# Performance work log

Hardware: AMD Instinct MI355X
Metric: run time of the kernel (lower is better)

## Reference

```python
import jax, jax.numpy as jnp
import numpy as np

N = 50000
E = 1600000
IN = 128
HID = 128
OUT = 64
NL = 200000
NEG_SLOPE = 0.2


def _glorot(key, shape):
    fan_in, fan_out = shape[0], shape[-1]
    s = jnp.sqrt(6.0 / (fan_in + fan_out))
    return jax.random.uniform(key, shape, jnp.float32, -s, s)


def setup_inputs() -> dict:
    key = jax.random.key(0)
    ks = jax.random.split(key, 16)
    x = jax.random.normal(ks[0], (N, IN), jnp.float32)
    edge_index = jax.random.randint(ks[1], (2, E), 0, N, dtype=jnp.int32)
    edge_label_index = jax.random.randint(ks[2], (2, NL), 0, N, dtype=jnp.int32)
    return {
        "x": x,
        "edge_index": edge_index,
        "edge_label_index": edge_label_index,
        "W1": _glorot(ks[3], (IN, HID)),  "a1s": _glorot(ks[4], (HID,)),  "a1d": _glorot(ks[5], (HID,)),  "b1": jnp.zeros((HID,), jnp.float32),
        "W2": _glorot(ks[6], (HID, HID)), "a2s": _glorot(ks[7], (HID,)),  "a2d": _glorot(ks[8], (HID,)),  "b2": jnp.zeros((HID,), jnp.float32),
        "W3": _glorot(ks[9], (HID, HID)), "a3s": _glorot(ks[10], (HID,)), "a3d": _glorot(ks[11], (HID,)), "b3": jnp.zeros((HID,), jnp.float32),
        "W4": _glorot(ks[12], (HID, OUT)), "b4": jnp.zeros((OUT,), jnp.float32),
    }


def _add_self_loops(edge_index, n):
    loop = jnp.arange(n, dtype=edge_index.dtype)
    return jnp.concatenate([edge_index, jnp.stack([loop, loop])], axis=1)


def gat_conv(x, edge_index, W, a_s, a_d, b):
    """PyG GATConv, heads=1, add_self_loops=True: gather, LeakyReLU score,
    segment softmax over destination nodes, scatter-add aggregate."""
    n = x.shape[0]
    ei = _add_self_loops(edge_index, n)
    src, dst = ei[0], ei[1]
    h = x @ W                                    # [N, H]
    e = jax.nn.leaky_relu((h @ a_s)[src] + (h @ a_d)[dst], NEG_SLOPE)  # [E']
    m = jax.ops.segment_max(e, dst, num_segments=n)
    p = jnp.exp(e - m[dst])
    s = jax.ops.segment_sum(p, dst, num_segments=n)
    alpha = p / s[dst]                           # segment softmax
    out = jax.ops.segment_sum(h[src] * alpha[:, None], dst, num_segments=n)
    return out + b


def gcn_conv(x, edge_index, W, b):
    """PyG GCNConv: self-loops + symmetric degree normalization."""
    n = x.shape[0]
    ei = _add_self_loops(edge_index, n)
    src, dst = ei[0], ei[1]
    h = x @ W
    deg = jax.ops.segment_sum(jnp.ones(src.shape, h.dtype), dst, num_segments=n)
    dinv = jax.lax.rsqrt(deg)
    norm = dinv[src] * dinv[dst]                 # [E']
    out = jax.ops.segment_sum(h[src] * norm[:, None], dst, num_segments=n)
    return out + b


def reference(x, edge_index, edge_label_index,
              W1, a1s, a1d, b1, W2, a2s, a2d, b2,
              W3, a3s, a3d, b3, W4, b4):
    h = jax.nn.relu(gat_conv(x, edge_index, W1, a1s, a1d, b1))
    h = jax.nn.relu(gat_conv(h, edge_index, W2, a2s, a2d, b2))
    h = jax.nn.relu(gat_conv(h, edge_index, W3, a3s, a3d, b3))
    z = gcn_conv(h, edge_index, W4, b4)          # [N, OUT]
    # decode: dot product of endpoint embeddings -> link logits [NL]
    return (z[edge_label_index[0]] * z[edge_label_index[1]]).sum(axis=-1)
```

## Files before the change

kernel.cpp:

```cpp
#include <hip/hip_runtime.h>
#include <hip/hip_fp16.h>
#include <math.h>

#define NN   50000
#define NE   1600000
#define DHID 128
#define DOUTC 64
#define NLBL 200000
#define CAP  80
#define NEG  0.2f
#define NBK  196
#define CAPB 8800
#define CHK  4096

typedef unsigned short u16;
typedef _Float16 half8 __attribute__((ext_vector_type(8)));
typedef float floatx4 __attribute__((ext_vector_type(4)));


__global__ __launch_bounds__(256) void k_zero(int* __restrict__ gcnt) {
    int i = threadIdx.x;
    if (i < NBK) gcnt[i] = 0;
}

__global__ __launch_bounds__(256) void k_bin(const int* __restrict__ ei,
                                             int* __restrict__ gcnt,
                                             unsigned* __restrict__ bins) {
    __shared__ int cntL[NBK];
    __shared__ int curL[NBK];
    const int tid = threadIdx.x;
    const int e0 = blockIdx.x * CHK + tid * 16;
    const bool act = (e0 + 15) < NE;

    unsigned pk[16];
    int bb[16];
    if (act) {
#pragma unroll
        for (int g = 0; g < 4; ++g) {
            int4 s4 = *(const int4*)&ei[e0 + g * 4];
            int4 d4 = *(const int4*)&ei[NE + e0 + g * 4];
            int sa[4] = {s4.x, s4.y, s4.z, s4.w};
            int da[4] = {d4.x, d4.y, d4.z, d4.w};
#pragma unroll
            for (int k = 0; k < 4; ++k) {
                int idx = g * 4 + k;
                bb[idx] = da[k] >> 8;
                pk[idx] = (unsigned)sa[k] | ((unsigned)(da[k] & 255) << 16);
            }
        }
    }
    for (int i = tid; i < NBK; i += 256) cntL[i] = 0;
    __syncthreads();
    if (act) {
#pragma unroll
        for (int k = 0; k < 16; ++k) atomicAdd(&cntL[bb[k]], 1);
    }
    __syncthreads();
    for (int i = tid; i < NBK; i += 256) curL[i] = atomicAdd(&gcnt[i], cntL[i]);
    __syncthreads();
    if (act) {
#pragma unroll
        for (int k = 0; k < 16; ++k) {
            int off = atomicAdd(&curL[bb[k]], 1);
            bins[(size_t)bb[k] * CAPB + off] = pk[k];
        }
    }
}

__global__ __launch_bounds__(256) void k_build(const unsigned* __restrict__ bins,
                                               const int* __restrict__ gcnt,
                                               int* __restrict__ cnt,
                                               u16* __restrict__ csr) {
    __shared__ u16 rows[256 * CAP];
    __shared__ int cur[256];
    const int b = blockIdx.x, tid = threadIdx.x;
    const int d0 = b << 8;
    const int nd = min(256, NN - d0);
    if (tid < nd) { cur[tid] = 1; rows[tid * CAP] = (u16)(d0 + tid); }
    __syncthreads();
    const int n = gcnt[b];
    for (int i = tid; i < n; i += 256) {
        unsigned v = bins[(size_t)b * CAPB + i];
        int s = v & 0xFFFF, dl = v >> 16;
        int pos = atomicAdd(&cur[dl], 1);
        if (pos < CAP) rows[dl * CAP + pos] = (u16)s;
    }
    __syncthreads();
    const unsigned* rw = (const unsigned*)rows;
    unsigned* cw = (unsigned*)(csr + (size_t)d0 * CAP);
    const int tot = nd * (CAP / 2);
    for (int i = tid; i < tot; i += 256) cw[i] = rw[i];
    if (tid < nd) cnt[d0 + tid] = cur[tid];
}


__global__ __launch_bounds__(256) void k_cast(const float* __restrict__ x,
                                              __half* __restrict__ x16) {
    int i = (blockIdx.x * 256 + threadIdx.x) * 4;
    if (i < NN * 128) {
        float4 v = *(const float4*)&x[i];
        __half2 h0 = __floats2half2_rn(v.x, v.y);
        __half2 h1 = __floats2half2_rn(v.z, v.w);
        uint2 u;
        __builtin_memcpy(&u.x, &h0, 4);
        __builtin_memcpy(&u.y, &h1, 4);
        *(uint2*)&x16[i] = u;
    }
}


template <int NOUT, bool ATTN>
__global__ __launch_bounds__(256) void gemm_mfma(const __half* __restrict__ A16,
                                                 const float* __restrict__ W,
                                                 __half* __restrict__ C16,
                                                 const float* __restrict__ a_s,
                                                 const float* __restrict__ a_d,
                                                 float* __restrict__ asv,
                                                 float* __restrict__ adv, int M) {
    constexpr int CT = NOUT / 16;
    __shared__ _Float16 Wt[NOUT][136];
    const int tid = threadIdx.x;
    for (int i4 = tid; i4 < 128 * NOUT / 4; i4 += 256) {
        int i = i4 * 4;
        int k = i / NOUT, n = i % NOUT;
        float4 w = *(const float4*)&W[i];
        Wt[n + 0][k] = (_Float16)w.x;
        Wt[n + 1][k] = (_Float16)w.y;
        Wt[n + 2][k] = (_Float16)w.z;
        Wt[n + 3][k] = (_Float16)w.w;
    }
    __syncthreads();

    const int wave = tid >> 6, lane = tid & 63;
    const int n = lane & 15, quad = lane >> 4;
    const int row0 = blockIdx.x * 64 + wave * 16;

    half8 a[4];
    const bool rowok = (row0 + n) < M;
    const _Float16* Ap = (const _Float16*)A16 + (size_t)(row0 + n) * 128 + quad * 8;
    half8 zz = {};
#pragma unroll
    for (int ks = 0; ks < 4; ++ks)
        a[ks] = rowok ? *(const half8*)(Ap + ks * 32) : zz;

    floatx4 acc[CT];
#pragma unroll
    for (int c = 0; c < CT; ++c) acc[c] = (floatx4){0.f, 0.f, 0.f, 0.f};

#pragma unroll
    for (int c = 0; c < CT; ++c) {
#pragma unroll
        for (int ks = 0; ks < 4; ++ks) {
            half8 b = *(const half8*)&Wt[c * 16 + n][ks * 32 + quad * 8];
            acc[c] = __builtin_amdgcn_mfma_f32_16x16x32_f16(a[ks], b, acc[c], 0, 0, 0);
        }
    }

#pragma unroll
    for (int c = 0; c < CT; ++c) {
#pragma unroll
        for (int reg = 0; reg < 4; ++reg) {
            int row = row0 + quad * 4 + reg;
            if (row < M) C16[(size_t)row * NOUT + c * 16 + n] = __float2half(acc[c][reg]);
        }
    }

    if (ATTN) {
        float ps[4] = {0.f, 0.f, 0.f, 0.f};
        float pd[4] = {0.f, 0.f, 0.f, 0.f};
#pragma unroll
        for (int c = 0; c < CT; ++c) {
            float sv = a_s[c * 16 + n];
            float dv = a_d[c * 16 + n];
#pragma unroll
            for (int reg = 0; reg < 4; ++reg) {
                ps[reg] = fmaf(acc[c][reg], sv, ps[reg]);
                pd[reg] = fmaf(acc[c][reg], dv, pd[reg]);
            }
        }
#pragma unroll
        for (int off = 1; off < 16; off <<= 1) {
#pragma unroll
            for (int reg = 0; reg < 4; ++reg) {
                ps[reg] += __shfl_xor(ps[reg], off);
                pd[reg] += __shfl_xor(pd[reg], off);
            }
        }
        if (n == 0) {
#pragma unroll
            for (int reg = 0; reg < 4; ++reg) {
                int row = row0 + quad * 4 + reg;
                if (row < M) { asv[row] = ps[reg]; adv[row] = pd[reg]; }
            }
        }
    }
}

__device__ inline void fma_h8(uint4 u, float al, float* acc) {
    float2 f0 = __half22float2(*(__half2*)&u.x);
    float2 f1 = __half22float2(*(__half2*)&u.y);
    float2 f2 = __half22float2(*(__half2*)&u.z);
    float2 f3 = __half22float2(*(__half2*)&u.w);
    acc[0] = fmaf(al, f0.x, acc[0]);
    acc[1] = fmaf(al, f0.y, acc[1]);
    acc[2] = fmaf(al, f1.x, acc[2]);
    acc[3] = fmaf(al, f1.y, acc[3]);
    acc[4] = fmaf(al, f2.x, acc[4]);
    acc[5] = fmaf(al, f2.y, acc[5]);
    acc[6] = fmaf(al, f3.x, acc[6]);
    acc[7] = fmaf(al, f3.y, acc[7]);
}


__global__ __launch_bounds__(256) void k_gat_agg(const __half* __restrict__ h,
                                                 const int* __restrict__ cnt,
                                                 const u16* __restrict__ csr,
                                                 const float* __restrict__ asv,
                                                 const float* __restrict__ adv,
                                                 const float* __restrict__ bias,
                                                 __half* __restrict__ outp) {
    int lane = threadIdx.x & 63, wv = threadIdx.x >> 6;
    int d = blockIdx.x * 4 + wv;
    if (d >= NN) return;
    int deg = cnt[d]; if (deg > CAP) deg = CAP;
    const float advd = adv[d];
    const u16* rowp = csr + (size_t)d * CAP;

    int j0 = lane, j1 = lane + 64;
    int s0 = 0, s1 = 0;
    float e0 = -INFINITY, e1 = -INFINITY;
    if (j0 < deg) {
        s0 = rowp[j0];
        float t = asv[s0] + advd;
        e0 = (t >= 0.f) ? t : NEG * t;
    }
    if (j1 < deg) {
        s1 = rowp[j1];
        float t = asv[s1] + advd;
        e1 = (t >= 0.f) ? t : NEG * t;
    }
    float m = fmaxf(e0, e1);
#pragma unroll
    for (int off = 32; off; off >>= 1) m = fmaxf(m, __shfl_xor(m, off));
    float p0 = (j0 < deg) ? __expf(e0 - m) : 0.f;
    float p1 = (j1 < deg) ? __expf(e1 - m) : 0.f;
    float s = p0 + p1;
#pragma unroll
    for (int off = 32; off; off >>= 1) s += __shfl_xor(s, off);
    float inv = 1.f / s;
    float a0 = p0 * inv, a1 = p1 * inv;

    int slot = lane >> 3, r = lane & 7;
    float acc[16];
#pragma unroll
    for (int k = 0; k < 16; ++k) acc[k] = 0.f;

    for (int base = 0; base < deg; base += 8) {
        int idx = base + slot;
        int lsrc = idx & 63;
        float alA = __shfl(a0, lsrc);
        float alB = __shfl(a1, lsrc);
        int   sjA = __shfl(s0, lsrc);
        int   sjB = __shfl(s1, lsrc);
        bool ok = idx < deg;
        float al = ok ? ((idx < 64) ? alA : alB) : 0.f;
        int   sj = ok ? ((idx < 64) ? sjA : sjB) : 0;
        const uint4* hp = (const uint4*)&h[(size_t)sj * 128 + r * 16];
        uint4 ua = hp[0];
        uint4 ub = hp[1];
        fma_h8(ua, al, acc);
        fma_h8(ub, al, acc + 8);
    }
#pragma unroll
    for (int k = 0; k < 16; ++k) {
        acc[k] += __shfl_xor(acc[k], 8);
        acc[k] += __shfl_xor(acc[k], 16);
        acc[k] += __shfl_xor(acc[k], 32);
    }
    if (slot == 0) {
        __half2 ho[8];
#pragma unroll
        for (int k = 0; k < 8; ++k) {
            float oa = fmaxf(acc[2 * k]     + bias[r * 16 + 2 * k],     0.f);
            float ob = fmaxf(acc[2 * k + 1] + bias[r * 16 + 2 * k + 1], 0.f);
            ho[k] = __floats2half2_rn(oa, ob);
        }
        uint4 u0, u1;
        __builtin_memcpy(&u0, &ho[0], 16);
        __builtin_memcpy(&u1, &ho[4], 16);
        uint4* op = (uint4*)&outp[(size_t)d * 128 + r * 16];
        op[0] = u0; op[1] = u1;
    }
}


__global__ __launch_bounds__(256) void k_gcn_agg(const __half* __restrict__ h,
                                                 const int* __restrict__ cnt,
                                                 const u16* __restrict__ csr,
                                                 const float* __restrict__ bias,
                                                 float* __restrict__ z) {
    int lane = threadIdx.x & 63, wv = threadIdx.x >> 6;
    int d = blockIdx.x * 4 + wv;
    if (d >= NN) return;
    int degc = cnt[d];
    int deg = degc > CAP ? CAP : degc;
    float did = rsqrtf((float)degc);
    const u16* rowp = csr + (size_t)d * CAP;

    int j0 = lane, j1 = lane + 64;
    int s0 = 0, s1 = 0;
    float n0 = 0.f, n1 = 0.f;
    if (j0 < deg) { s0 = rowp[j0]; n0 = rsqrtf((float)cnt[s0]) * did; }
    if (j1 < deg) { s1 = rowp[j1]; n1 = rsqrtf((float)cnt[s1]) * did; }

    int slot = lane >> 3, r = lane & 7;
    float acc[8];
#pragma unroll
    for (int k = 0; k < 8; ++k) acc[k] = 0.f;

    for (int base = 0; base < deg; base += 8) {
        int idx = base + slot;
        int lsrc = idx & 63;
        float nA = __shfl(n0, lsrc);
        float nB = __shfl(n1, lsrc);
        int  sjA = __shfl(s0, lsrc);
        int  sjB = __shfl(s1, lsrc);
        bool ok = idx < deg;
        float nm = ok ? ((idx < 64) ? nA : nB) : 0.f;
        int   sj = ok ? ((idx < 64) ? sjA : sjB) : 0;
        uint4 u = *(const uint4*)&h[(size_t)sj * 64 + r * 8];
        fma_h8(u, nm, acc);
    }
#pragma unroll
    for (int k = 0; k < 8; ++k) {
        acc[k] += __shfl_xor(acc[k], 8);
        acc[k] += __shfl_xor(acc[k], 16);
        acc[k] += __shfl_xor(acc[k], 32);
    }
    if (slot == 0) {
        float4 b0 = *(const float4*)&bias[r * 8];
        float4 b1 = *(const float4*)&bias[r * 8 + 4];
        float4* zp = (float4*)&z[(size_t)d * 64 + r * 8];
        zp[0] = make_float4(acc[0] + b0.x, acc[1] + b0.y, acc[2] + b0.z, acc[3] + b0.w);
        zp[1] = make_float4(acc[4] + b1.x, acc[5] + b1.y, acc[6] + b1.z, acc[7] + b1.w);
    }
}


__global__ __launch_bounds__(256) void k_decode(const float* __restrict__ z,
                                                const int* __restrict__ eli,
                                                float* __restrict__ outp) {
    int lane = threadIdx.x & 63, wv = threadIdx.x >> 6;
    int g = lane >> 4, r = lane & 15;
    int idx = (blockIdx.x * 4 + wv) * 4 + g;
    if (idx >= NLBL) return;
    int a = eli[idx], b = eli[NLBL + idx];
    float4 za = *(const float4*)&z[(size_t)a * 64 + r * 4];
    float4 zb = *(const float4*)&z[(size_t)b * 64 + r * 4];
    float v = za.x * zb.x + za.y * zb.y + za.z * zb.z + za.w * zb.w;
#pragma unroll
    for (int off = 8; off; off >>= 1) v += __shfl_xor(v, off);
    if (r == 0) outp[idx] = v;
}


extern "C" void kernel_launch(void* const* d_in, const int* in_sizes, int n_in,
                              void* d_out, int out_size, void* d_ws, size_t ws_size,
                              hipStream_t stream) {
    const float* x   = (const float*)d_in[0];
    const int*   ei  = (const int*)d_in[1];
    const int*   eli = (const int*)d_in[2];
    const float* W1 = (const float*)d_in[3];
    const float* a1s = (const float*)d_in[4];
    const float* a1d = (const float*)d_in[5];
    const float* b1 = (const float*)d_in[6];
    const float* W2 = (const float*)d_in[7];
    const float* a2s = (const float*)d_in[8];
    const float* a2d = (const float*)d_in[9];
    const float* b2 = (const float*)d_in[10];
    const float* W3 = (const float*)d_in[11];
    const float* a3s = (const float*)d_in[12];
    const float* a3d = (const float*)d_in[13];
    const float* b3 = (const float*)d_in[14];
    const float* W4 = (const float*)d_in[15];
    const float* b4 = (const float*)d_in[16];
    float* outp = (float*)d_out;

    char* p = (char*)d_ws;
    auto alloc = [&](size_t bytes) -> char* {
        char* r = p;
        p += (bytes + 255) & ~(size_t)255;
        return r;
    };
    int*    cnt  = (int*)alloc((size_t)NN * 4);
    u16*    csr  = (u16*)alloc((size_t)NN * CAP * 2);
    int*    gcnt = (int*)alloc((size_t)NBK * 4);
    float*  asv  = (float*)alloc((size_t)NN * 4);
    float*  advv = (float*)alloc((size_t)NN * 4);
    __half* x16  = (__half*)alloc((size_t)NN * 128 * 2);
    __half* G    = (__half*)alloc((size_t)NN * 128 * 2);
    __half* Bu1  = (__half*)alloc((size_t)NN * 128 * 2);
    __half* Bu2  = (__half*)alloc((size_t)NN * 128 * 2);
    float*  zf   = (float*)alloc((size_t)NN * 64 * 4);
    unsigned* bins = (unsigned*)alloc((size_t)NBK * CAPB * 4);

    const int gBin  = (NE + CHK - 1) / CHK;
    const int gCast = (NN * 128 / 4 + 255) / 256;
    const int gGemm = (NN + 63) / 64;
    const int gNode = (NN + 3) / 4;
    const int gDec  = (NLBL + 15) / 16;

    k_zero<<<1, 256, 0, stream>>>(gcnt);
    k_bin<<<gBin, 256, 0, stream>>>(ei, gcnt, bins);
    k_build<<<NBK, 256, 0, stream>>>(bins, gcnt, cnt, csr);
    k_cast<<<gCast, 256, 0, stream>>>(x, x16);

    gemm_mfma<128, true><<<gGemm, 256, 0, stream>>>(x16, W1, G, a1s, a1d, asv, advv, NN);
    k_gat_agg<<<gNode, 256, 0, stream>>>(G, cnt, csr, asv, advv, b1, Bu1);

    gemm_mfma<128, true><<<gGemm, 256, 0, stream>>>(Bu1, W2, G, a2s, a2d, asv, advv, NN);
    k_gat_agg<<<gNode, 256, 0, stream>>>(G, cnt, csr, asv, advv, b2, Bu2);

    gemm_mfma<128, true><<<gGemm, 256, 0, stream>>>(Bu2, W3, G, a3s, a3d, asv, advv, NN);
    k_gat_agg<<<gNode, 256, 0, stream>>>(G, cnt, csr, asv, advv, b3, Bu1);

    gemm_mfma<64, false><<<gGemm, 256, 0, stream>>>(Bu1, W4, G, nullptr, nullptr, nullptr, nullptr, NN);
    k_gcn_agg<<<gNode, 256, 0, stream>>>(G, cnt, csr, b4, zf);

    k_decode<<<gDec, 256, 0, stream>>>(zf, eli, outp);
}
```

Before: 444.1 us.

## Pre-pack weights into MFMA fragment layout and double rows per wave in GEMM

```diff
diff --git a/kernel.cpp b/kernel.cpp
--- a/kernel.cpp
+++ b/kernel.cpp
@@ -109,89 +109,108 @@
 }
 
 
+__global__ __launch_bounds__(256) void k_prep_w(const float* __restrict__ W1f,
+                                                const float* __restrict__ W2f,
+                                                const float* __restrict__ W3f,
+                                                const float* __restrict__ W4f,
+                                                half8* __restrict__ Wf1,
+                                                half8* __restrict__ Wf2,
+                                                half8* __restrict__ Wf3,
+                                                half8* __restrict__ Wf4) {
+    int e = blockIdx.x * 256 + threadIdx.x;
+    const float* W;
+    half8* Wf;
+    int nout, le;
+    if (e < 2048)      { W = W1f; Wf = Wf1; nout = 128; le = e; }
+    else if (e < 4096) { W = W2f; Wf = Wf2; nout = 128; le = e - 2048; }
+    else if (e < 6144) { W = W3f; Wf = Wf3; nout = 128; le = e - 4096; }
+    else if (e < 7168) { W = W4f; Wf = Wf4; nout = 64;  le = e - 6144; }
+    else return;
+    int c = le >> 8, rem = le & 255, ks = rem >> 6, lane = rem & 63;
+    int n = lane & 15, quad = lane >> 4;
+    int col = c * 16 + n, k0 = ks * 32 + quad * 8;
+    half8 v;
+#pragma unroll
+    for (int j = 0; j < 8; ++j) v[j] = (_Float16)W[(size_t)(k0 + j) * nout + col];
+    Wf[le] = v;
+}
+
+
 template <int NOUT, bool ATTN>
 __global__ __launch_bounds__(256) void gemm_mfma(const __half* __restrict__ A16,
-                                                 const float* __restrict__ W,
+                                                 const half8* __restrict__ Wf,
                                                  __half* __restrict__ C16,
                                                  const float* __restrict__ a_s,
                                                  const float* __restrict__ a_d,
                                                  float* __restrict__ asv,
                                                  float* __restrict__ adv, int M) {
     constexpr int CT = NOUT / 16;
-    __shared__ _Float16 Wt[NOUT][136];
     const int tid = threadIdx.x;
-    for (int i4 = tid; i4 < 128 * NOUT / 4; i4 += 256) {
-        int i = i4 * 4;
-        int k = i / NOUT, n = i % NOUT;
-        float4 w = *(const float4*)&W[i];
-        Wt[n + 0][k] = (_Float16)w.x;
-        Wt[n + 1][k] = (_Float16)w.y;
-        Wt[n + 2][k] = (_Float16)w.z;
-        Wt[n + 3][k] = (_Float16)w.w;
-    }
-    __syncthreads();
-
     const int wave = tid >> 6, lane = tid & 63;
     const int n = lane & 15, quad = lane >> 4;
-    const int row0 = blockIdx.x * 64 + wave * 16;
-
-    half8 a[4];
-    const bool rowok = (row0 + n) < M;
-    const _Float16* Ap = (const _Float16*)A16 + (size_t)(row0 + n) * 128 + quad * 8;
+    const int row0 = blockIdx.x * 128 + wave * 32;
+
+    half8 a[2][4];
     half8 zz = {};
 #pragma unroll
-    for (int ks = 0; ks < 4; ++ks)
-        a[ks] = rowok ? *(const half8*)(Ap + ks * 32) : zz;
-
-    floatx4 acc[CT];
-#pragma unroll
-    for (int c = 0; c < CT; ++c) acc[c] = (floatx4){0.f, 0.f, 0.f, 0.f};
+    for (int t = 0; t < 2; ++t) {
+        int row = row0 + t * 16 + n;
+        const _Float16* Ap = (const _Float16*)A16 + (size_t)row * 128 + quad * 8;
+        bool ok = row < M;
+#pragma unroll
+        for (int ks = 0; ks < 4; ++ks)
+            a[t][ks] = ok ? *(const half8*)(Ap + ks * 32) : zz;
+    }
+
+    floatx4 acc[2][CT];
+#pragma unroll
+    for (int t = 0; t < 2; ++t)
+#pragma unroll
+        for (int c = 0; c < CT; ++c) acc[t][c] = (floatx4){0.f, 0.f, 0.f, 0.f};
 
 #pragma unroll
     for (int c = 0; c < CT; ++c) {
 #pragma unroll
         for (int ks = 0; ks < 4; ++ks) {
-            half8 b = *(const half8*)&Wt[c * 16 + n][ks * 32 + quad * 8];
-            acc[c] = __builtin_amdgcn_mfma_f32_16x16x32_f16(a[ks], b, acc[c], 0, 0, 0);
-        }
-    }
-
-#pragma unroll
-    for (int c = 0; c < CT; ++c) {
-#pragma unroll
-        for (int reg = 0; reg < 4; ++reg) {
-            int row = row0 + quad * 4 + reg;
-            if (row < M) C16[(size_t)row * NOUT + c * 16 + n] = __float2half(acc[c][reg]);
+            half8 b = Wf[(c * 4 + ks) * 64 + lane];
+            acc[0][c] = __builtin_amdgcn_mfma_f32_16x16x32_f16(b, a[0][ks], acc[0][c], 0, 0, 0);
+            acc[1][c] = __builtin_amdgcn_mfma_f32_16x16x32_f16(b, a[1][ks], acc[1][c], 0, 0, 0);
+        }
+    }
+
+#pragma unroll
+    for (int t = 0; t < 2; ++t) {
+        int row = row0 + t * 16 + n;
+        if (row < M) {
+#pragma unroll
+            for (int c = 0; c < CT; ++c) {
+                __half2 h0 = __floats2half2_rn(acc[t][c][0], acc[t][c][1]);
+                __half2 h1 = __floats2half2_rn(acc[t][c][2], acc[t][c][3]);
+                uint2 u;
+                __builtin_memcpy(&u.x, &h0, 4);
+                __builtin_memcpy(&u.y, &h1, 4);
+                *(uint2*)&C16[(size_t)row * NOUT + c * 16 + quad * 4] = u;
+            }
         }
     }
 
     if (ATTN) {
-        float ps[4] = {0.f, 0.f, 0.f, 0.f};
-        float pd[4] = {0.f, 0.f, 0.f, 0.f};
-#pragma unroll
-        for (int c = 0; c < CT; ++c) {
-            float sv = a_s[c * 16 + n];
-            float dv = a_d[c * 16 + n];
-#pragma unroll
-            for (int reg = 0; reg < 4; ++reg) {
-                ps[reg] = fmaf(acc[c][reg], sv, ps[reg]);
-                pd[reg] = fmaf(acc[c][reg], dv, pd[reg]);
+#pragma unroll
+        for (int t = 0; t < 2; ++t) {
+            float ps = 0.f, pd = 0.f;
+#pragma unroll
+            for (int c = 0; c < CT; ++c) {
+#pragma unroll
+                for (int reg = 0; reg < 4; ++reg) {
+                    float w = acc[t][c][reg];
+                    ps = fmaf(w, a_s[c * 16 + quad * 4 + reg], ps);
+                    pd = fmaf(w, a_d[c * 16 + quad * 4 + reg], pd);
+                }
             }
-        }
-#pragma unroll
-        for (int off = 1; off < 16; off <<= 1) {
-#pragma unroll
-            for (int reg = 0; reg < 4; ++reg) {
-                ps[reg] += __shfl_xor(ps[reg], off);
-                pd[reg] += __shfl_xor(pd[reg], off);
-            }
-        }
-        if (n == 0) {
-#pragma unroll
-            for (int reg = 0; reg < 4; ++reg) {
-                int row = row0 + quad * 4 + reg;
-                if (row < M) { asv[row] = ps[reg]; adv[row] = pd[reg]; }
-            }
+            ps += __shfl_xor(ps, 16); ps += __shfl_xor(ps, 32);
+            pd += __shfl_xor(pd, 16); pd += __shfl_xor(pd, 32);
+            int row = row0 + t * 16 + n;
+            if (quad == 0 && row < M) { asv[row] = ps; adv[row] = pd; }
         }
     }
 }
@@ -402,11 +421,15 @@
     __half* Bu1  = (__half*)alloc((size_t)NN * 128 * 2);
     __half* Bu2  = (__half*)alloc((size_t)NN * 128 * 2);
     float*  zf   = (float*)alloc((size_t)NN * 64 * 4);
+    half8*  Wf1  = (half8*)alloc(2048 * 16);
+    half8*  Wf2  = (half8*)alloc(2048 * 16);
+    half8*  Wf3  = (half8*)alloc(2048 * 16);
+    half8*  Wf4  = (half8*)alloc(1024 * 16);
     unsigned* bins = (unsigned*)alloc((size_t)NBK * CAPB * 4);
 
     const int gBin  = (NE + CHK - 1) / CHK;
     const int gCast = (NN * 128 / 4 + 255) / 256;
-    const int gGemm = (NN + 63) / 64;
+    const int gGemm = (NN + 127) / 128;
     const int gNode = (NN + 3) / 4;
     const int gDec  = (NLBL + 15) / 16;
 
@@ -414,17 +437,18 @@
     k_bin<<<gBin, 256, 0, stream>>>(ei, gcnt, bins);
     k_build<<<NBK, 256, 0, stream>>>(bins, gcnt, cnt, csr);
     k_cast<<<gCast, 256, 0, stream>>>(x, x16);
-
-    gemm_mfma<128, true><<<gGemm, 256, 0, stream>>>(x16, W1, G, a1s, a1d, asv, advv, NN);
+    k_prep_w<<<28, 256, 0, stream>>>(W1, W2, W3, W4, Wf1, Wf2, Wf3, Wf4);
+
+    gemm_mfma<128, true><<<gGemm, 256, 0, stream>>>(x16, Wf1, G, a1s, a1d, asv, advv, NN);
     k_gat_agg<<<gNode, 256, 0, stream>>>(G, cnt, csr, asv, advv, b1, Bu1);
 
-    gemm_mfma<128, true><<<gGemm, 256, 0, stream>>>(Bu1, W2, G, a2s, a2d, asv, advv, NN);
+    gemm_mfma<128, true><<<gGemm, 256, 0, stream>>>(Bu1, Wf2, G, a2s, a2d, asv, advv, NN);
     k_gat_agg<<<gNode, 256, 0, stream>>>(G, cnt, csr, asv, advv, b2, Bu2);
 
-    gemm_mfma<128, true><<<gGemm, 256, 0, stream>>>(Bu2, W3, G, a3s, a3d, asv, advv, NN);
+    gemm_mfma<128, true><<<gGemm, 256, 0, stream>>>(Bu2, Wf3, G, a3s, a3d, asv, advv, NN);
     k_gat_agg<<<gNode, 256, 0, stream>>>(G, cnt, csr, asv, advv, b3, Bu1);
 
-    gemm_mfma<64, false><<<gGemm, 256, 0, stream>>>(Bu1, W4, G, nullptr, nullptr, nullptr, nullptr, NN);
+    gemm_mfma<64, false><<<gGemm, 256, 0, stream>>>(Bu1, Wf4, G, nullptr, nullptr, nullptr, nullptr, NN);
     k_gcn_agg<<<gNode, 256, 0, stream>>>(G, cnt, csr, b4, zf);
 
     k_decode<<<gDec, 256, 0, stream>>>(zf, eli, outp);
```

Measured after the change: 430.2 us. -3.1%, faster.
